# Kernel tuning notes

Hardware: AMD Instinct MI355X
Metric: run time of the kernel (lower is better)

## Reference

```python
import jax, jax.numpy as jnp
import numpy as np

B, S, H_SZ = 1, 2048, 2048
E, K, KVH, D = 8, 2, 16, 128      # experts, top_k, kv heads, head_dim
QH = K * KVH                       # 32 query heads
QSZ = KVH * D                      # 2048 per-expert q/o size


def setup_inputs() -> dict:
    key = jax.random.key(0)
    ks = jax.random.split(key, 6)
    hidden_states = jax.random.normal(ks[0], (B, S, H_SZ), jnp.float32)
    causal = jnp.tril(jnp.ones((S, S), dtype=bool))
    attention_bias = jnp.where(causal, 0.0, -1e9).astype(jnp.float32)[None, None]  # [1,1,S,S]
    inv_freq = 1.0 / (10000.0 ** (jnp.arange(0, D, 2, dtype=jnp.float32) / D))     # [D/2]
    ang = jnp.arange(S, dtype=jnp.float32)[:, None] * inv_freq[None, :]            # [S,D/2]
    cos, sin = jnp.cos(ang), jnp.sin(ang)
    router_w = jax.random.normal(ks[1], (E, H_SZ), jnp.float32) * 0.02
    q_w = jax.random.normal(ks[2], (E, QSZ, H_SZ), jnp.float32) * 0.02
    o_w = jax.random.normal(ks[3], (E, H_SZ, QSZ), jnp.float32) * 0.02
    kv_w = jax.random.normal(ks[4], (2 * QSZ, H_SZ), jnp.float32) * 0.02
    bias = jax.random.normal(ks[5], (H_SZ,), jnp.float32) * 0.02
    return {"hidden_states": hidden_states, "attention_bias": attention_bias,
            "cos": cos, "sin": sin, "router_w": router_w, "q_w": q_w,
            "o_w": o_w, "kv_w": kv_w, "bias": bias}


def _rope(x, cos, sin):
    # x: [b,s,h,d]; half-rotation rotary, cos/sin: [s,d/2]
    d2 = x.shape[-1] // 2
    x1, x2 = x[..., :d2], x[..., d2:]
    c = cos[None, :, None, :]
    s = sin[None, :, None, :]
    return jnp.concatenate([x1 * c - x2 * s, x1 * s + x2 * c], axis=-1)


def reference(hidden_states, attention_bias, cos, sin, router_w, q_w, o_w, kv_w, bias):
    # ---- router: top-k + softmax over top-k logits ----
    logits = jnp.einsum('bsh,eh->bse', hidden_states, router_w)         # [b,s,E]
    top_vals, sel = jax.lax.top_k(logits, K)                            # [b,s,K]
    gates = jax.nn.softmax(top_vals, axis=-1)                           # [b,s,K]
    # ---- per-expert Q projections (dense, as in original), gather selected ----
    q_all = jnp.einsum('bsh,eqh->bseq', hidden_states, q_w)             # [b,s,E,QSZ]
    q_sel = jnp.take_along_axis(q_all, sel[..., None], axis=2)          # [b,s,K,QSZ]
    # slots -> kv-major head layout: [b,s,K,KVH,D] -> [b,s,KVH,K,D] -> [b,s,QH,D]
    q = q_sel.reshape(B, S, K, KVH, D).transpose(0, 1, 3, 2, 4).reshape(B, S, QH, D)
    # ---- shared K/V ----
    kv = jnp.einsum('bsh,oh->bso', hidden_states, kv_w)                 # [b,s,2*QSZ]
    k_st, v_st = jnp.split(kv, 2, axis=-1)
    k_st = k_st.reshape(B, S, KVH, D)
    v_st = v_st.reshape(B, S, KVH, D)
    # ---- rotary ----
    q = _rope(q, cos, sin)
    k_st = _rope(k_st, cos, sin)
    # ---- GQA attention (group size K; kv-major query layout matches repeat) ----
    k_rep = jnp.repeat(k_st, K, axis=2)                                 # [b,s,QH,D]
    v_rep = jnp.repeat(v_st, K, axis=2)
    scale = D ** -0.5
    scores = jnp.einsum('bqhd,bkhd->bhqk', q, k_rep) * scale + attention_bias
    probs = jax.nn.softmax(scores, axis=-1)
    attn = jnp.einsum('bhqk,bkhd->bqhd', probs, v_rep)                  # [b,s,QH,D]
    # back to slot-major: [b,s,KVH,K,D] -> [b,s,K,KVH,D] -> [b,s,K,QSZ]
    attn4 = attn.reshape(B, S, KVH, K, D).transpose(0, 1, 3, 2, 4).reshape(B, S, K, QSZ)
    # ---- per-expert O projections, masked + gated sum (as in original) ----
    out = jnp.zeros((B, S, H_SZ), hidden_states.dtype)
    for e in range(E):
        o_e = jnp.einsum('bskq,hq->bskh', attn4, o_w[e])                # [b,s,K,H]
        m = (sel == e).astype(hidden_states.dtype) * gates              # [b,s,K]
        out = out + jnp.einsum('bsk,bskh->bsh', m, o_e)
    return out + bias
```

## Files before the change

kernel.cpp:

```cpp
#include <hip/hip_runtime.h>
#include <hip/hip_bf16.h>
#include <stdint.h>

#define S_LEN 2048
#define HSZ 2048
#define NE 8
#define TOPK 2
#define NKVH 16
#define HD 128
#define NQH 32
#define QSZ 2048

typedef __attribute__((ext_vector_type(8))) __bf16 bf16x8;
typedef __attribute__((ext_vector_type(4))) float f32x4;

#define BM 128
#define BN 128
#define BK 64

__device__ __forceinline__ void gload_lds16(const void* g, void* l) {
  __builtin_amdgcn_global_load_lds((__attribute__((address_space(1))) void*)g,
                                   (__attribute__((address_space(3))) void*)l, 16, 0, 0);
}

__device__ __forceinline__ bf16x8 pack8(float4 a, float4 b) {
  bf16x8 r;
  r[0] = (__bf16)a.x; r[1] = (__bf16)a.y; r[2] = (__bf16)a.z; r[3] = (__bf16)a.w;
  r[4] = (__bf16)b.x; r[5] = (__bf16)b.y; r[6] = (__bf16)b.z; r[7] = (__bf16)b.w;
  return r;
}

__global__ __launch_bounds__(256) void cast_kernel(const float* __restrict__ src,
                                                   __bf16* __restrict__ dst, long n) {
  long i0 = ((long)blockIdx.x * 256 + threadIdx.x) * 4;
  long stride = (long)gridDim.x * 256 * 4;
  for (long i = i0; i < n; i += stride) {
    float4 v = *(const float4*)(src + i);
    unsigned short a = __builtin_bit_cast(unsigned short, (__bf16)v.x);
    unsigned short b = __builtin_bit_cast(unsigned short, (__bf16)v.y);
    unsigned short c = __builtin_bit_cast(unsigned short, (__bf16)v.z);
    unsigned short d = __builtin_bit_cast(unsigned short, (__bf16)v.w);
    uint2 o;
    o.x = (unsigned)a | ((unsigned)b << 16);
    o.y = (unsigned)c | ((unsigned)d << 16);
    *(uint2*)(dst + i) = o;
  }
}

__global__ __launch_bounds__(256) void router_kernel(const float* __restrict__ hs,
                                                     const float* __restrict__ rw,
                                                     int* __restrict__ sel,
                                                     float* __restrict__ gates) {
  const int s = blockIdx.x * 4 + (threadIdx.x >> 6);
  const int lane = threadIdx.x & 63;
  const float* row = hs + (size_t)s * HSZ;
  float acc[NE];
#pragma unroll
  for (int e = 0; e < NE; ++e) acc[e] = 0.f;
  for (int j = lane; j < HSZ; j += 64) {
    float x = row[j];
#pragma unroll
    for (int e = 0; e < NE; ++e) acc[e] += x * rw[e * HSZ + j];
  }
#pragma unroll
  for (int e = 0; e < NE; ++e) {
#pragma unroll
    for (int off = 32; off > 0; off >>= 1) acc[e] += __shfl_xor(acc[e], off);
  }
  if (lane == 0) {
    int i0 = 0; float v0 = acc[0];
#pragma unroll
    for (int e = 1; e < NE; ++e) if (acc[e] > v0) { v0 = acc[e]; i0 = e; }
    int i1 = -1; float v1 = -1e30f;
#pragma unroll
    for (int e = 0; e < NE; ++e) if (e != i0 && acc[e] > v1) { v1 = acc[e]; i1 = e; }
    float ge = __expf(v1 - v0);
    float den = 1.f + ge;
    sel[s * 2] = i0; sel[s * 2 + 1] = i1;
    gates[s * 2] = 1.f / den; gates[s * 2 + 1] = ge / den;
  }
}

__global__ void bucket_kernel(const int* __restrict__ sel, int* __restrict__ pair_list,
                              int* __restrict__ expert_off) {
  __shared__ int cnt[NE], base[NE];
  const int t = threadIdx.x;
  if (t < NE) cnt[t] = 0;
  __syncthreads();
  for (int p2 = t; p2 < S_LEN * TOPK; p2 += 256) atomicAdd(&cnt[sel[p2]], 1);
  __syncthreads();
  if (t == 0) {
    int run = 0;
#pragma unroll
    for (int e = 0; e < NE; ++e) { base[e] = run; expert_off[e] = run; run += cnt[e]; }
    expert_off[NE] = run;
  }
  __syncthreads();
  for (int p2 = t; p2 < S_LEN * TOPK; p2 += 256) {
    int pos = atomicAdd(&base[sel[p2]], 1);
    pair_list[pos] = p2;
  }
}

template <int MODE>
__global__ __launch_bounds__(256) void gemm_kernel(const __bf16* __restrict__ A_src,
                                                   const float* __restrict__ B_src,
                                                   const int* __restrict__ pair_list,
                                                   const int* __restrict__ expert_off,
                                                   const float* __restrict__ gates,
                                                   __bf16* __restrict__ out_bf,
                                                   __bf16* __restrict__ out_vT,
                                                   float* __restrict__ out_f32) {
  constexpr int KD = 2048;
  constexpr int NT = KD / BK;
  const int n0 = blockIdx.x * BN;
  const int m0 = blockIdx.y * BM;
  const int e = blockIdx.z;
  int start = 0, cntv = S_LEN;
  if constexpr (MODE != 0) {
    start = expert_off[e];
    cntv = expert_off[e + 1] - start;
    if (m0 >= cntv) return;
  }
  const float* Bb = B_src + (size_t)e * QSZ * HSZ;
  __shared__ __attribute__((aligned(16))) __bf16 As[2][BM * BK];
  __shared__ __attribute__((aligned(16))) __bf16 Bs[2][BN * BK];
  __shared__ const __bf16* a_rows[BM];
  __shared__ int row_pair[BM];
  const int t = threadIdx.x;
  if (t < BM) {
    if constexpr (MODE == 0) {
      a_rows[t] = A_src + (size_t)(m0 + t) * KD;
      row_pair[t] = 0;
    } else {
      int idx = m0 + t;
      bool valid = idx < cntv;
      int pp = pair_list[start + (valid ? idx : 0)];
      row_pair[t] = valid ? pp : -1;
      size_t arow = (MODE == 1) ? (size_t)(pp >> 1) : (size_t)pp;
      a_rows[t] = A_src + arow * (size_t)KD;
    }
  }
  __syncthreads();

  const int lane = t & 63, w = t >> 6;
  const int wr = (w >> 1) * 64, wc = (w & 1) * 64;
  const int lr = lane & 15, g = lane >> 4;
  const int xa = lr & 7;

  const __bf16* a_srow[4];
  int a_soff[4];
#pragma unroll
  for (int i = 0; i < 4; ++i) {
    const int c = t + i * 256;
    const int row = c >> 3, win = c & 7;
    a_srow[i] = a_rows[row];
    a_soff[i] = (win ^ (row & 7)) * 8;
  }

  const int brow = t >> 2;
  const int bq = t & 3;
  const float* bp0 = Bb + (size_t)(n0 + brow) * KD + bq * 16;
  const float* bp1 = bp0 + (size_t)64 * KD;
  const int c0 = (2 * bq) ^ (brow & 7);
  const int c1 = (2 * bq + 1) ^ (brow & 7);
  const int bo00 = brow * BK + c0 * 8, bo01 = brow * BK + c1 * 8;
  const int bo10 = (brow + 64) * BK + c0 * 8, bo11 = (brow + 64) * BK + c1 * 8;

  f32x4 acc[4][4];
#pragma unroll
  for (int m = 0; m < 4; ++m)
#pragma unroll
    for (int n = 0; n < 4; ++n) acc[m][n] = (f32x4)0.f;

#pragma unroll
  for (int i = 0; i < 4; ++i)
    gload_lds16(a_srow[i] + a_soff[i], (char*)As[0] + (t + i * 256) * 16);
  float4 cA0 = *(const float4*)(bp0), cA1 = *(const float4*)(bp0 + 4);
  float4 cA2 = *(const float4*)(bp0 + 8), cA3 = *(const float4*)(bp0 + 12);
  float4 cB0 = *(const float4*)(bp1), cB1 = *(const float4*)(bp1 + 4);
  float4 cB2 = *(const float4*)(bp1 + 8), cB3 = *(const float4*)(bp1 + 12);

#pragma unroll 2
  for (int ti = 0; ti < NT; ++ti) {
    const int cur = ti & 1;
    *(bf16x8*)(&Bs[cur][bo00]) = pack8(cA0, cA1);
    *(bf16x8*)(&Bs[cur][bo01]) = pack8(cA2, cA3);
    *(bf16x8*)(&Bs[cur][bo10]) = pack8(cB0, cB1);
    *(bf16x8*)(&Bs[cur][bo11]) = pack8(cB2, cB3);
    __syncthreads();

    if (ti + 1 < NT) {
      const int k1 = (ti + 1) * BK;
#pragma unroll
      for (int i = 0; i < 4; ++i)
        gload_lds16(a_srow[i] + k1 + a_soff[i], (char*)As[cur ^ 1] + (t + i * 256) * 16);
      cA0 = *(const float4*)(bp0 + k1); cA1 = *(const float4*)(bp0 + k1 + 4);
      cA2 = *(const float4*)(bp0 + k1 + 8); cA3 = *(const float4*)(bp0 + k1 + 12);
      cB0 = *(const float4*)(bp1 + k1); cB1 = *(const float4*)(bp1 + k1 + 4);
      cB2 = *(const float4*)(bp1 + k1 + 8); cB3 = *(const float4*)(bp1 + k1 + 12);
    }
    __builtin_amdgcn_sched_barrier(0);

#pragma unroll
    for (int kk = 0; kk < BK; kk += 32) {
      bf16x8 af[4], bfv[4];
#pragma unroll
      for (int m = 0; m < 4; ++m)
        af[m] = *(const bf16x8*)(&As[cur][(wr + m * 16 + lr) * BK + (((kk >> 3) + g) ^ xa) * 8]);
#pragma unroll
      for (int n = 0; n < 4; ++n)
        bfv[n] = *(const bf16x8*)(&Bs[cur][(wc + n * 16 + lr) * BK + (((kk >> 3) + g) ^ xa) * 8]);
#pragma unroll
      for (int m = 0; m < 4; ++m)
#pragma unroll
        for (int n = 0; n < 4; ++n)
          acc[m][n] = __builtin_amdgcn_mfma_f32_16x16x32_bf16(af[m], bfv[n], acc[m][n], 0, 0, 0);
    }
    __builtin_amdgcn_sched_barrier(0);
  }

  const int lg = lane >> 4;
  if constexpr (MODE == 0) {
    if (n0 < 2048) {
#pragma unroll
      for (int m = 0; m < 4; ++m)
#pragma unroll
        for (int r = 0; r < 4; ++r) {
          const int row = wr + m * 16 + lg * 4 + r;
#pragma unroll
          for (int n = 0; n < 4; ++n) {
            const int col = n0 + wc + n * 16 + lr;
            out_bf[(size_t)(m0 + row) * 2048 + col] = (__bf16)acc[m][n][r];
          }
        }
    } else {
#pragma unroll
      for (int m = 0; m < 4; ++m) {
        const int sb = m0 + wr + m * 16 + lg * 4;
#pragma unroll
        for (int n = 0; n < 4; ++n) {
          const int cv = n0 + wc + n * 16 + lr - 2048;
          uint2 pk;
          unsigned short h0 = __builtin_bit_cast(unsigned short, (__bf16)acc[m][n][0]);
          unsigned short h1 = __builtin_bit_cast(unsigned short, (__bf16)acc[m][n][1]);
          unsigned short h2 = __builtin_bit_cast(unsigned short, (__bf16)acc[m][n][2]);
          unsigned short h3 = __builtin_bit_cast(unsigned short, (__bf16)acc[m][n][3]);
          pk.x = (unsigned)h0 | ((unsigned)h1 << 16);
          pk.y = (unsigned)h2 | ((unsigned)h3 << 16);
          *(uint2*)(out_vT + (size_t)cv * S_LEN + sb) = pk;
        }
      }
    }
  } else {
#pragma unroll
    for (int m = 0; m < 4; ++m) {
#pragma unroll
      for (int r = 0; r < 4; ++r) {
        const int row = wr + m * 16 + lg * 4 + r;
        const int pp = row_pair[row];
        if (pp < 0) continue;
        if constexpr (MODE == 1) {
#pragma unroll
          for (int n = 0; n < 4; ++n) {
            const int col = n0 + wc + n * 16 + lr;
            out_bf[(size_t)pp * QSZ + col] = (__bf16)acc[m][n][r];
          }
        } else {
          const float gt = gates[pp];
#pragma unroll
          for (int n = 0; n < 4; ++n) {
            const int col = n0 + wc + n * 16 + lr;
            out_f32[(size_t)pp * HSZ + col] = acc[m][n][r] * gt;
          }
        }
      }
    }
  }
}

__global__ __launch_bounds__(256) void rope_q_kernel(const __bf16* __restrict__ q_lin,
                                                     const float* __restrict__ cosb,
                                                     const float* __restrict__ sinb,
                                                     __bf16* __restrict__ q_attn) {
  const int idx = blockIdx.x * 4 + (threadIdx.x >> 6);
  const int lane = threadIdx.x & 63;
  const int s = idx >> 5;
  const int h = idx & 31;
  const int kvh = h >> 1, k = h & 1;
  const __bf16* src = q_lin + ((size_t)s * 2 + k) * QSZ + kvh * HD;
  float x1 = (float)src[lane];
  float x2 = (float)src[lane + 64];
  float c = cosb[s * 64 + lane], sn = sinb[s * 64 + lane];
  __bf16* dst = q_attn + ((size_t)h * S_LEN + s) * HD;
  dst[lane] = (__bf16)(x1 * c - x2 * sn);
  dst[lane + 64] = (__bf16)(x1 * sn + x2 * c);
}

__global__ __launch_bounds__(256) void rope_k_kernel(const __bf16* __restrict__ kv_lin,
                                                     const float* __restrict__ cosb,
                                                     const float* __restrict__ sinb,
                                                     __bf16* __restrict__ k_attn) {
  const int idx = blockIdx.x * 4 + (threadIdx.x >> 6);
  const int lane = threadIdx.x & 63;
  const int s = idx >> 4;
  const int gq = idx & 15;
  const __bf16* ksrc = kv_lin + (size_t)s * 2048 + gq * HD;
  float x1 = (float)ksrc[lane], x2 = (float)ksrc[lane + 64];
  float c = cosb[s * 64 + lane], sn = sinb[s * 64 + lane];
  __bf16* kd = k_attn + ((size_t)gq * S_LEN + s) * HD;
  kd[lane] = (__bf16)(x1 * c - x2 * sn);
  kd[lane + 64] = (__bf16)(x1 * sn + x2 * c);
}

__global__ __launch_bounds__(256, 2) void attn_kernel(const __bf16* __restrict__ q_attn,
                                                      const __bf16* __restrict__ k_attn,
                                                      const __bf16* __restrict__ vT,
                                                      __bf16* __restrict__ attn4) {
  __shared__ __attribute__((aligned(16))) __bf16 Ks[2][64 * 128];
  __shared__ __attribute__((aligned(16))) __bf16 Vs[2][128 * 64];
  const int h = blockIdx.x;
  const int by = (blockIdx.y < 8) ? blockIdx.y : 23 - blockIdx.y;
  const int s0 = by * 128;
  const int t = threadIdx.x;
  const int lane = t & 63;
  const int w = t >> 6;
  const int g = lane >> 4;
  const int lr = lane & 15;
  const int kvh = h >> 1;

  int koff[4], voff[4];
#pragma unroll
  for (int i = 0; i < 4; ++i) {
    const int c = t + i * 256;
    const int kvL = c >> 4, w16 = c & 15;
    koff[i] = kvL * HD + ((w16 ^ (kvL & 7)) * 8);
    const int d = c >> 3, w8 = c & 7;
    voff[i] = d * S_LEN + ((w8 ^ (d & 7)) * 8);
  }
  const __bf16* Kb = k_attn + (size_t)kvh * S_LEN * HD;
  const __bf16* Vb = vT + (size_t)kvh * HD * S_LEN;

  auto stage = [&](int buf, int kv0) {
#pragma unroll
    for (int i = 0; i < 4; ++i) {
      const int c = t + i * 256;
      gload_lds16(Kb + (size_t)kv0 * HD + koff[i], (char*)Ks[buf] + c * 16);
      gload_lds16(Vb + (size_t)kv0 + voff[i], (char*)Vs[buf] + c * 16);
    }
  };

  bf16x8 qf[2][4];
#pragma unroll
  for (int m = 0; m < 2; ++m) {
    const __bf16* qbase = q_attn + ((size_t)h * S_LEN + s0 + w * 32 + m * 16 + lr) * HD;
#pragma unroll
    for (int ds = 0; ds < 4; ++ds) qf[m][ds] = *(const bf16x8*)(qbase + ds * 32 + g * 8);
  }

  float m_run[2] = {-1e30f, -1e30f}, l_run[2] = {0.f, 0.f};
  f32x4 acc[2][8];
#pragma unroll
  for (int m = 0; m < 2; ++m)
#pragma unroll
    for (int dt = 0; dt < 8; ++dt) acc[m][dt] = (f32x4)0.f;

  const int xr = (lr & 7) << 4;
  const int nt = 2 * by + 2;
  stage(0, 0);
  for (int ti = 0; ti < nt; ++ti) {
    const int cur = ti & 1;
    const int kv0 = ti * 64;
    __syncthreads();
    if (ti + 1 < nt) stage(cur ^ 1, kv0 + 64);

    f32x4 sc[2][4];
#pragma unroll
    for (int m = 0; m < 2; ++m)
#pragma unroll
      for (int b = 0; b < 4; ++b) sc[m][b] = (f32x4)0.f;
#pragma unroll
    for (int b = 0; b < 4; ++b) {
#pragma unroll
      for (int ds = 0; ds < 4; ++ds) {
        const bf16x8 kf = *(const bf16x8*)((const char*)Ks[cur] +
            (b * 16 + lr) * 256 + ((ds * 64 + g * 16) ^ xr));
        sc[0][b] = __builtin_amdgcn_mfma_f32_16x16x32_bf16(kf, qf[0][ds], sc[0][b], 0, 0, 0);
        sc[1][b] = __builtin_amdgcn_mfma_f32_16x16x32_bf16(kf, qf[1][ds], sc[1][b], 0, 0, 0);
      }
    }

    bf16x8 paf[2][2];
#pragma unroll
    for (int m = 0; m < 2; ++m) {
      const int qrow = s0 + w * 32 + m * 16 + lr;
      float p[4][4];
      float tmax = -1e30f;
#pragma unroll
      for (int b = 0; b < 4; ++b)
#pragma unroll
        for (int r = 0; r < 4; ++r) {
          const int kv = kv0 + b * 16 + g * 4 + r;
          float v = sc[m][b][r] * 0.08838834764831845f;
          if (kv > qrow) v = -1e30f;
          p[b][r] = v;
          tmax = fmaxf(tmax, v);
        }
      tmax = fmaxf(tmax, __shfl_xor(tmax, 16));
      tmax = fmaxf(tmax, __shfl_xor(tmax, 32));
      const float m_new = fmaxf(m_run[m], tmax);
      const float alpha = __expf(m_run[m] - m_new);
      float lsum = 0.f;
#pragma unroll
      for (int b = 0; b < 4; ++b)
#pragma unroll
        for (int r = 0; r < 4; ++r) {
          p[b][r] = __expf(p[b][r] - m_new);
          lsum += p[b][r];
        }
      lsum += __shfl_xor(lsum, 16);
      lsum += __shfl_xor(lsum, 32);
      l_run[m] = l_run[m] * alpha + lsum;
      m_run[m] = m_new;

      float ar[4];
#pragma unroll
      for (int r = 0; r < 4; ++r) ar[r] = __shfl(alpha, g * 4 + r);
#pragma unroll
      for (int dt = 0; dt < 8; ++dt)
#pragma unroll
        for (int r = 0; r < 4; ++r) acc[m][dt][r] *= ar[r];

#pragma unroll
      for (int half = 0; half < 2; ++half) {
        bf16x8 af;
#pragma unroll
        for (int j = 0; j < 8; ++j) {
          const int srcl = lr + 16 * ((g & 1) * 2 + (j >> 2));
          const float va = __shfl(p[half * 2][j & 3], srcl);
          const float vb = __shfl(p[half * 2 + 1][j & 3], srcl);
          af[j] = (__bf16)((g >> 1) ? vb : va);
        }
        paf[m][half] = af;
      }
    }

#pragma unroll
    for (int dt = 0; dt < 8; ++dt) {
      const char* vrow = (const char*)Vs[cur] + (dt * 16 + lr) * 128;
      const bf16x8 v0 = *(const bf16x8*)(vrow + ((g * 16) ^ xr));
      const bf16x8 v1 = *(const bf16x8*)(vrow + ((64 + g * 16) ^ xr));
      acc[0][dt] = __builtin_amdgcn_mfma_f32_16x16x32_bf16(paf[0][0], v0, acc[0][dt], 0, 0, 0);
      acc[0][dt] = __builtin_amdgcn_mfma_f32_16x16x32_bf16(paf[0][1], v1, acc[0][dt], 0, 0, 0);
      acc[1][dt] = __builtin_amdgcn_mfma_f32_16x16x32_bf16(paf[1][0], v0, acc[1][dt], 0, 0, 0);
      acc[1][dt] = __builtin_amdgcn_mfma_f32_16x16x32_bf16(paf[1][1], v1, acc[1][dt], 0, 0, 0);
    }
  }

#pragma unroll
  for (int m = 0; m < 2; ++m) {
    const float li = 1.f / l_run[m];
    float linv[4];
#pragma unroll
    for (int r = 0; r < 4; ++r) linv[r] = __shfl(li, g * 4 + r);
#pragma unroll
    for (int dt = 0; dt < 8; ++dt)
#pragma unroll
      for (int r = 0; r < 4; ++r) {
        const int qg = s0 + w * 32 + m * 16 + g * 4 + r;
        attn4[((size_t)qg * 2 + (h & 1)) * QSZ + kvh * HD + dt * 16 + lr] =
            (__bf16)(acc[m][dt][r] * linv[r]);
      }
  }
}

__global__ __launch_bounds__(256) void final_kernel(const float* __restrict__ o_tmp,
                                                    const float* __restrict__ bias,
                                                    float* __restrict__ out) {
  const size_t i = ((size_t)blockIdx.x * 256 + threadIdx.x) * 4;
  const int s = (int)(i >> 11);
  const int hcol = (int)(i & 2047);
  float4 a = *(const float4*)(o_tmp + ((size_t)s * 2) * HSZ + hcol);
  float4 b = *(const float4*)(o_tmp + ((size_t)s * 2 + 1) * HSZ + hcol);
  float4 bb = *(const float4*)(bias + hcol);
  float4 o;
  o.x = a.x + b.x + bb.x; o.y = a.y + b.y + bb.y;
  o.z = a.z + b.z + bb.z; o.w = a.w + b.w + bb.w;
  *(float4*)(out + i) = o;
}

extern "C" void kernel_launch(void* const* d_in, const int* in_sizes, int n_in,
                              void* d_out, int out_size, void* d_ws, size_t ws_size,
                              hipStream_t stream) {
  (void)in_sizes; (void)n_in; (void)out_size; (void)ws_size;
  const float* hs = (const float*)d_in[0];
  const float* cosb = (const float*)d_in[2];
  const float* sinb = (const float*)d_in[3];
  const float* rw = (const float*)d_in[4];
  const float* qw = (const float*)d_in[5];
  const float* ow = (const float*)d_in[6];
  const float* kvw = (const float*)d_in[7];
  const float* bias = (const float*)d_in[8];
  float* outp = (float*)d_out;

  char* base = (char*)d_ws;
  size_t off = 0;
  auto take = [&](size_t bytes) {
    char* r = base + off;
    off += (bytes + 255) & ~(size_t)255;
    return r;
  };
  __bf16* hid_bf  = (__bf16*)take((size_t)S_LEN * HSZ * 2);
  __bf16* k_attn  = (__bf16*)take((size_t)NKVH * S_LEN * HD * 2);
  __bf16* v_attnT = (__bf16*)take((size_t)NKVH * HD * S_LEN * 2);
  char* bufA = take((size_t)S_LEN * 4096 * 2);
  char* bufBC = take((size_t)S_LEN * TOPK * HSZ * 4);
  int* sel = (int*)take((size_t)S_LEN * TOPK * 4);
  float* gates = (float*)take((size_t)S_LEN * TOPK * 4);
  int* pair_list = (int*)take((size_t)S_LEN * TOPK * 4);
  int* expert_off = (int*)take((size_t)(NE + 1) * 4);

  __bf16* kv_lin = (__bf16*)bufA;
  __bf16* attn4 = (__bf16*)bufA;
  __bf16* q_lin = (__bf16*)bufBC;
  __bf16* q_attn = (__bf16*)(bufBC + (size_t)16 * 1024 * 1024);
  float* o_tmp = (float*)bufBC;

  cast_kernel<<<1024, 256, 0, stream>>>(hs, hid_bf, (long)S_LEN * HSZ);
  router_kernel<<<S_LEN / 4, 256, 0, stream>>>(hs, rw, sel, gates);
  bucket_kernel<<<1, 256, 0, stream>>>(sel, pair_list, expert_off);
  gemm_kernel<0><<<dim3(4096 / BN, S_LEN / BM, 1), 256, 0, stream>>>(
      hid_bf, kvw, nullptr, nullptr, nullptr, kv_lin, v_attnT, nullptr);
  rope_k_kernel<<<S_LEN * NKVH / 4, 256, 0, stream>>>(kv_lin, cosb, sinb, k_attn);
  gemm_kernel<1><<<dim3(QSZ / BN, 32, NE), 256, 0, stream>>>(
      hid_bf, qw, pair_list, expert_off, nullptr, q_lin, nullptr, nullptr);
  rope_q_kernel<<<S_LEN * NQH / 4, 256, 0, stream>>>(q_lin, cosb, sinb, q_attn);
  attn_kernel<<<dim3(NQH, 16), 256, 0, stream>>>(q_attn, k_attn, v_attnT, attn4);
  gemm_kernel<2><<<dim3(HSZ / BN, 32, NE), 256, 0, stream>>>(
      attn4, ow, pair_list, expert_off, gates, nullptr, nullptr, o_tmp);
  final_kernel<<<(S_LEN * HSZ / 4) / 256, 256, 0, stream>>>(o_tmp, bias, outp);
}
```

Measured before the change: 428.8 us.

## Prefetch B tiles two stages ahead with explicit vmcnt waits in GEMM

Restructures the GEMM main loop so the fp32 B tiles are loaded into registers two K-steps ahead, using two register sets in a manually unrolled pair of steps. The bf16 A tile is still staged directly into LDS one step ahead. Explicit s_waitcnt vmcnt counts ensure only the data needed for the current tile has landed, and a raw s_barrier replaces __syncthreads. The kernel also gets a launch-bounds hint of two blocks per CU. The aim is to hide global-load latency behind the MFMA work, at the cost of more register pressure and fragile hand-counted wait values.

```diff
diff --git a/kernel.cpp b/kernel.cpp
--- a/kernel.cpp
+++ b/kernel.cpp
@@ -103,14 +103,14 @@
 }
 
 template <int MODE>
-__global__ __launch_bounds__(256) void gemm_kernel(const __bf16* __restrict__ A_src,
-                                                   const float* __restrict__ B_src,
-                                                   const int* __restrict__ pair_list,
-                                                   const int* __restrict__ expert_off,
-                                                   const float* __restrict__ gates,
-                                                   __bf16* __restrict__ out_bf,
-                                                   __bf16* __restrict__ out_vT,
-                                                   float* __restrict__ out_f32) {
+__global__ __launch_bounds__(256, 2) void gemm_kernel(const __bf16* __restrict__ A_src,
+                                                      const float* __restrict__ B_src,
+                                                      const int* __restrict__ pair_list,
+                                                      const int* __restrict__ expert_off,
+                                                      const float* __restrict__ gates,
+                                                      __bf16* __restrict__ out_bf,
+                                                      __bf16* __restrict__ out_vT,
+                                                      float* __restrict__ out_f32) {
   constexpr int KD = 2048;
   constexpr int NT = KD / BK;
   const int n0 = blockIdx.x * BN;
@@ -173,35 +173,12 @@
 #pragma unroll
     for (int n = 0; n < 4; ++n) acc[m][n] = (f32x4)0.f;
 
-#pragma unroll
-  for (int i = 0; i < 4; ++i)
-    gload_lds16(a_srow[i] + a_soff[i], (char*)As[0] + (t + i * 256) * 16);
-  float4 cA0 = *(const float4*)(bp0), cA1 = *(const float4*)(bp0 + 4);
-  float4 cA2 = *(const float4*)(bp0 + 8), cA3 = *(const float4*)(bp0 + 12);
-  float4 cB0 = *(const float4*)(bp1), cB1 = *(const float4*)(bp1 + 4);
-  float4 cB2 = *(const float4*)(bp1 + 8), cB3 = *(const float4*)(bp1 + 12);
-
-#pragma unroll 2
-  for (int ti = 0; ti < NT; ++ti) {
-    const int cur = ti & 1;
-    *(bf16x8*)(&Bs[cur][bo00]) = pack8(cA0, cA1);
-    *(bf16x8*)(&Bs[cur][bo01]) = pack8(cA2, cA3);
-    *(bf16x8*)(&Bs[cur][bo10]) = pack8(cB0, cB1);
-    *(bf16x8*)(&Bs[cur][bo11]) = pack8(cB2, cB3);
-    __syncthreads();
-
-    if (ti + 1 < NT) {
-      const int k1 = (ti + 1) * BK;
-#pragma unroll
-      for (int i = 0; i < 4; ++i)
-        gload_lds16(a_srow[i] + k1 + a_soff[i], (char*)As[cur ^ 1] + (t + i * 256) * 16);
-      cA0 = *(const float4*)(bp0 + k1); cA1 = *(const float4*)(bp0 + k1 + 4);
-      cA2 = *(const float4*)(bp0 + k1 + 8); cA3 = *(const float4*)(bp0 + k1 + 12);
-      cB0 = *(const float4*)(bp1 + k1); cB1 = *(const float4*)(bp1 + k1 + 4);
-      cB2 = *(const float4*)(bp1 + k1 + 8); cB3 = *(const float4*)(bp1 + k1 + 12);
-    }
-    __builtin_amdgcn_sched_barrier(0);
-
+  auto stageA = [&](int dstbuf, int k1) {
+#pragma unroll
+    for (int i = 0; i < 4; ++i)
+      gload_lds16(a_srow[i] + k1 + a_soff[i], (char*)As[dstbuf] + (t + i * 256) * 16);
+  };
+  auto mfma_tile = [&](int cur) {
 #pragma unroll
     for (int kk = 0; kk < BK; kk += 32) {
       bf16x8 af[4], bfv[4];
@@ -217,8 +194,46 @@
         for (int n = 0; n < 4; ++n)
           acc[m][n] = __builtin_amdgcn_mfma_f32_16x16x32_bf16(af[m], bfv[n], acc[m][n], 0, 0, 0);
     }
-    __builtin_amdgcn_sched_barrier(0);
-  }
+  };
+
+#define B_LOAD8(S0, S1, S2, S3, S4, S5, S6, S7, KB)                          \
+  S0 = *(const float4*)(bp0 + (KB));      S1 = *(const float4*)(bp0 + (KB) + 4);  \
+  S2 = *(const float4*)(bp0 + (KB) + 8);  S3 = *(const float4*)(bp0 + (KB) + 12); \
+  S4 = *(const float4*)(bp1 + (KB));      S5 = *(const float4*)(bp1 + (KB) + 4);  \
+  S6 = *(const float4*)(bp1 + (KB) + 8);  S7 = *(const float4*)(bp1 + (KB) + 12);
+
+#define GEMM_STEP(TI, CUR, S0, S1, S2, S3, S4, S5, S6, S7)                   \
+  *(bf16x8*)(&Bs[CUR][bo00]) = pack8(S0, S1);                                \
+  *(bf16x8*)(&Bs[CUR][bo01]) = pack8(S2, S3);                                \
+  *(bf16x8*)(&Bs[CUR][bo10]) = pack8(S4, S5);                                \
+  *(bf16x8*)(&Bs[CUR][bo11]) = pack8(S6, S7);                                \
+  asm volatile("s_waitcnt lgkmcnt(0)" ::: "memory");                         \
+  __builtin_amdgcn_s_barrier();                                              \
+  if ((TI) + 2 < NT) { B_LOAD8(S0, S1, S2, S3, S4, S5, S6, S7, ((TI) + 2) * BK) } \
+  __builtin_amdgcn_sched_barrier(0);                                         \
+  if ((TI) + 1 < NT) stageA((CUR) ^ 1, ((TI) + 1) * BK);                     \
+  __builtin_amdgcn_sched_barrier(0);                                         \
+  if ((TI) + 2 < NT) { asm volatile("s_waitcnt vmcnt(12)" ::: "memory"); }   \
+  else if ((TI) + 1 < NT) { asm volatile("s_waitcnt vmcnt(4)" ::: "memory"); } \
+  else { asm volatile("s_waitcnt vmcnt(0)" ::: "memory"); }                  \
+  __builtin_amdgcn_sched_barrier(0);                                         \
+  mfma_tile(CUR);                                                            \
+  __builtin_amdgcn_sched_barrier(0);
+
+  float4 bA0, bA1, bA2, bA3, bA4, bA5, bA6, bA7;
+  float4 bB0, bB1, bB2, bB3, bB4, bB5, bB6, bB7;
+  B_LOAD8(bA0, bA1, bA2, bA3, bA4, bA5, bA6, bA7, 0)
+  B_LOAD8(bB0, bB1, bB2, bB3, bB4, bB5, bB6, bB7, BK)
+  __builtin_amdgcn_sched_barrier(0);
+  stageA(0, 0);
+  __builtin_amdgcn_sched_barrier(0);
+
+  for (int tb = 0; tb < NT; tb += 2) {
+    GEMM_STEP(tb, 0, bA0, bA1, bA2, bA3, bA4, bA5, bA6, bA7)
+    GEMM_STEP(tb + 1, 1, bB0, bB1, bB2, bB3, bB4, bB5, bB6, bB7)
+  }
+#undef GEMM_STEP
+#undef B_LOAD8
 
   const int lg = lane >> 4;
   if constexpr (MODE == 0) {
```

After: 435.7 us. Within noise of the previous version (+1.6%).

## Shrink GEMM N-tile and drop double buffering to raise occupancy

Applied to the files above, without the earlier changes.

The tiled GEMM kernel is reworked to use 128x64 output tiles, with four waves each owning 32 rows, instead of 128x128 tiles on a 2x2 wave grid. The LDS double buffer and the register prefetch of the next K-slice are removed in favour of a plain load, sync, compute, sync loop. Launch bounds now request 4 blocks per CU. The aim is higher occupancy and more blocks to hide latency. The cost is no explicit load/compute overlap and twice the re-reads of the A tile across N tiles. The MoE grid's y-dimension is trimmed to 16, the maximum number of 128-row tiles per expert.

```diff
diff --git a/kernel.cpp b/kernel.cpp
--- a/kernel.cpp
+++ b/kernel.cpp
@@ -15,7 +15,7 @@
 typedef __attribute__((ext_vector_type(4))) float f32x4;
 
 #define BM 128
-#define BN 128
+#define BN 64
 #define BK 64
 
 __device__ __forceinline__ void gload_lds16(const void* g, void* l) {
@@ -103,14 +103,14 @@
 }
 
 template <int MODE>
-__global__ __launch_bounds__(256) void gemm_kernel(const __bf16* __restrict__ A_src,
-                                                   const float* __restrict__ B_src,
-                                                   const int* __restrict__ pair_list,
-                                                   const int* __restrict__ expert_off,
-                                                   const float* __restrict__ gates,
-                                                   __bf16* __restrict__ out_bf,
-                                                   __bf16* __restrict__ out_vT,
-                                                   float* __restrict__ out_f32) {
+__global__ __launch_bounds__(256, 4) void gemm_kernel(const __bf16* __restrict__ A_src,
+                                                      const float* __restrict__ B_src,
+                                                      const int* __restrict__ pair_list,
+                                                      const int* __restrict__ expert_off,
+                                                      const float* __restrict__ gates,
+                                                      __bf16* __restrict__ out_bf,
+                                                      __bf16* __restrict__ out_vT,
+                                                      float* __restrict__ out_f32) {
   constexpr int KD = 2048;
   constexpr int NT = KD / BK;
   const int n0 = blockIdx.x * BN;
@@ -123,8 +123,8 @@
     if (m0 >= cntv) return;
   }
   const float* Bb = B_src + (size_t)e * QSZ * HSZ;
-  __shared__ __attribute__((aligned(16))) __bf16 As[2][BM * BK];
-  __shared__ __attribute__((aligned(16))) __bf16 Bs[2][BN * BK];
+  __shared__ __attribute__((aligned(16))) __bf16 As[BM * BK];
+  __shared__ __attribute__((aligned(16))) __bf16 Bs[BN * BK];
   __shared__ const __bf16* a_rows[BM];
   __shared__ int row_pair[BM];
   const int t = threadIdx.x;
@@ -144,7 +144,7 @@
   __syncthreads();
 
   const int lane = t & 63, w = t >> 6;
-  const int wr = (w >> 1) * 64, wc = (w & 1) * 64;
+  const int wr = w * 32;
   const int lr = lane & 15, g = lane >> 4;
   const int xa = lr & 7;
 
@@ -161,86 +161,70 @@
   const int brow = t >> 2;
   const int bq = t & 3;
   const float* bp0 = Bb + (size_t)(n0 + brow) * KD + bq * 16;
-  const float* bp1 = bp0 + (size_t)64 * KD;
   const int c0 = (2 * bq) ^ (brow & 7);
   const int c1 = (2 * bq + 1) ^ (brow & 7);
-  const int bo00 = brow * BK + c0 * 8, bo01 = brow * BK + c1 * 8;
-  const int bo10 = (brow + 64) * BK + c0 * 8, bo11 = (brow + 64) * BK + c1 * 8;
-
-  f32x4 acc[4][4];
-#pragma unroll
-  for (int m = 0; m < 4; ++m)
+  const int bo0 = brow * BK + c0 * 8, bo1 = brow * BK + c1 * 8;
+
+  f32x4 acc[2][4];
+#pragma unroll
+  for (int m = 0; m < 2; ++m)
 #pragma unroll
     for (int n = 0; n < 4; ++n) acc[m][n] = (f32x4)0.f;
 
-#pragma unroll
-  for (int i = 0; i < 4; ++i)
-    gload_lds16(a_srow[i] + a_soff[i], (char*)As[0] + (t + i * 256) * 16);
-  float4 cA0 = *(const float4*)(bp0), cA1 = *(const float4*)(bp0 + 4);
-  float4 cA2 = *(const float4*)(bp0 + 8), cA3 = *(const float4*)(bp0 + 12);
-  float4 cB0 = *(const float4*)(bp1), cB1 = *(const float4*)(bp1 + 4);
-  float4 cB2 = *(const float4*)(bp1 + 8), cB3 = *(const float4*)(bp1 + 12);
-
-#pragma unroll 2
   for (int ti = 0; ti < NT; ++ti) {
-    const int cur = ti & 1;
-    *(bf16x8*)(&Bs[cur][bo00]) = pack8(cA0, cA1);
-    *(bf16x8*)(&Bs[cur][bo01]) = pack8(cA2, cA3);
-    *(bf16x8*)(&Bs[cur][bo10]) = pack8(cB0, cB1);
-    *(bf16x8*)(&Bs[cur][bo11]) = pack8(cB2, cB3);
+    const int k0 = ti * BK;
+#pragma unroll
+    for (int i = 0; i < 4; ++i)
+      gload_lds16(a_srow[i] + k0 + a_soff[i], (char*)As + (t + i * 256) * 16);
+    {
+      float4 f0 = *(const float4*)(bp0 + k0);
+      float4 f1 = *(const float4*)(bp0 + k0 + 4);
+      float4 f2 = *(const float4*)(bp0 + k0 + 8);
+      float4 f3 = *(const float4*)(bp0 + k0 + 12);
+      *(bf16x8*)(&Bs[bo0]) = pack8(f0, f1);
+      *(bf16x8*)(&Bs[bo1]) = pack8(f2, f3);
+    }
     __syncthreads();
 
-    if (ti + 1 < NT) {
-      const int k1 = (ti + 1) * BK;
-#pragma unroll
-      for (int i = 0; i < 4; ++i)
-        gload_lds16(a_srow[i] + k1 + a_soff[i], (char*)As[cur ^ 1] + (t + i * 256) * 16);
-      cA0 = *(const float4*)(bp0 + k1); cA1 = *(const float4*)(bp0 + k1 + 4);
-      cA2 = *(const float4*)(bp0 + k1 + 8); cA3 = *(const float4*)(bp0 + k1 + 12);
-      cB0 = *(const float4*)(bp1 + k1); cB1 = *(const float4*)(bp1 + k1 + 4);
-      cB2 = *(const float4*)(bp1 + k1 + 8); cB3 = *(const float4*)(bp1 + k1 + 12);
-    }
-    __builtin_amdgcn_sched_barrier(0);
-
 #pragma unroll
     for (int kk = 0; kk < BK; kk += 32) {
-      bf16x8 af[4], bfv[4];
-#pragma unroll
-      for (int m = 0; m < 4; ++m)
-        af[m] = *(const bf16x8*)(&As[cur][(wr + m * 16 + lr) * BK + (((kk >> 3) + g) ^ xa) * 8]);
+      bf16x8 af[2], bfv[4];
+#pragma unroll
+      for (int m = 0; m < 2; ++m)
+        af[m] = *(const bf16x8*)(&As[(wr + m * 16 + lr) * BK + (((kk >> 3) + g) ^ xa) * 8]);
 #pragma unroll
       for (int n = 0; n < 4; ++n)
-        bfv[n] = *(const bf16x8*)(&Bs[cur][(wc + n * 16 + lr) * BK + (((kk >> 3) + g) ^ xa) * 8]);
-#pragma unroll
-      for (int m = 0; m < 4; ++m)
+        bfv[n] = *(const bf16x8*)(&Bs[(n * 16 + lr) * BK + (((kk >> 3) + g) ^ xa) * 8]);
+#pragma unroll
+      for (int m = 0; m < 2; ++m)
 #pragma unroll
         for (int n = 0; n < 4; ++n)
           acc[m][n] = __builtin_amdgcn_mfma_f32_16x16x32_bf16(af[m], bfv[n], acc[m][n], 0, 0, 0);
     }
-    __builtin_amdgcn_sched_barrier(0);
+    __syncthreads();
   }
 
   const int lg = lane >> 4;
   if constexpr (MODE == 0) {
     if (n0 < 2048) {
 #pragma unroll
-      for (int m = 0; m < 4; ++m)
+      for (int m = 0; m < 2; ++m)
 #pragma unroll
         for (int r = 0; r < 4; ++r) {
           const int row = wr + m * 16 + lg * 4 + r;
 #pragma unroll
           for (int n = 0; n < 4; ++n) {
-            const int col = n0 + wc + n * 16 + lr;
+            const int col = n0 + n * 16 + lr;
             out_bf[(size_t)(m0 + row) * 2048 + col] = (__bf16)acc[m][n][r];
           }
         }
     } else {
 #pragma unroll
-      for (int m = 0; m < 4; ++m) {
+      for (int m = 0; m < 2; ++m) {
         const int sb = m0 + wr + m * 16 + lg * 4;
 #pragma unroll
         for (int n = 0; n < 4; ++n) {
-          const int cv = n0 + wc + n * 16 + lr - 2048;
+          const int cv = n0 + n * 16 + lr - 2048;
           uint2 pk;
           unsigned short h0 = __builtin_bit_cast(unsigned short, (__bf16)acc[m][n][0]);
           unsigned short h1 = __builtin_bit_cast(unsigned short, (__bf16)acc[m][n][1]);
@@ -254,7 +238,7 @@
     }
   } else {
 #pragma unroll
-    for (int m = 0; m < 4; ++m) {
+    for (int m = 0; m < 2; ++m) {
 #pragma unroll
       for (int r = 0; r < 4; ++r) {
         const int row = wr + m * 16 + lg * 4 + r;
@@ -263,14 +247,14 @@
         if constexpr (MODE == 1) {
 #pragma unroll
           for (int n = 0; n < 4; ++n) {
-            const int col = n0 + wc + n * 16 + lr;
+            const int col = n0 + n * 16 + lr;
             out_bf[(size_t)pp * QSZ + col] = (__bf16)acc[m][n][r];
           }
         } else {
           const float gt = gates[pp];
 #pragma unroll
           for (int n = 0; n < 4; ++n) {
-            const int col = n0 + wc + n * 16 + lr;
+            const int col = n0 + n * 16 + lr;
             out_f32[(size_t)pp * HSZ + col] = acc[m][n][r] * gt;
           }
         }
@@ -532,11 +516,11 @@
   gemm_kernel<0><<<dim3(4096 / BN, S_LEN / BM, 1), 256, 0, stream>>>(
       hid_bf, kvw, nullptr, nullptr, nullptr, kv_lin, v_attnT, nullptr);
   rope_k_kernel<<<S_LEN * NKVH / 4, 256, 0, stream>>>(kv_lin, cosb, sinb, k_attn);
-  gemm_kernel<1><<<dim3(QSZ / BN, 32, NE), 256, 0, stream>>>(
+  gemm_kernel<1><<<dim3(QSZ / BN, 16, NE), 256, 0, stream>>>(
       hid_bf, qw, pair_list, expert_off, nullptr, q_lin, nullptr, nullptr);
   rope_q_kernel<<<S_LEN * NQH / 4, 256, 0, stream>>>(q_lin, cosb, sinb, q_attn);
   attn_kernel<<<dim3(NQH, 16), 256, 0, stream>>>(q_attn, k_attn, v_attnT, attn4);
-  gemm_kernel<2><<<dim3(HSZ / BN, 32, NE), 256, 0, stream>>>(
+  gemm_kernel<2><<<dim3(HSZ / BN, 16, NE), 256, 0, stream>>>(
       attn4, ow, pair_list, expert_off, gates, nullptr, nullptr, o_tmp);
   final_kernel<<<(S_LEN * HSZ / 4) / 256, 256, 0, stream>>>(o_tmp, bias, outp);
 }
```

Measured after the change: 463.3 us. +8.0%, slower.

## Merge KV and Q GEMMs into one launch, split-K the O GEMM, single-buffer LDS

Applied to the files above, without the earlier changes.

Fuses the KV projection and the per-expert Q projection GEMMs into a single launch with a flat block index, so both run concurrently and fill the device better. The O-projection GEMM is split along K into two halves that write gated bf16 partials, and the final kernel sums four partial rows plus bias. The GEMM main loops drop the register/LDS double-buffer prefetch in favor of a single LDS buffer with two barriers per tile, and launch_bounds request 4 blocks per CU for occupancy. The trade-off is losing load/compute overlap within a block, and bf16 partials reduce accuracy of the output accumulation.

```diff
diff --git a/kernel.cpp b/kernel.cpp
--- a/kernel.cpp
+++ b/kernel.cpp
@@ -102,34 +102,40 @@
   }
 }
 
-template <int MODE>
-__global__ __launch_bounds__(256) void gemm_kernel(const __bf16* __restrict__ A_src,
-                                                   const float* __restrict__ B_src,
-                                                   const int* __restrict__ pair_list,
-                                                   const int* __restrict__ expert_off,
-                                                   const float* __restrict__ gates,
-                                                   __bf16* __restrict__ out_bf,
-                                                   __bf16* __restrict__ out_vT,
-                                                   float* __restrict__ out_f32) {
+
+__global__ __launch_bounds__(256, 4) void gemm01_kernel(
+    const __bf16* __restrict__ A_src, const float* __restrict__ kvw,
+    const float* __restrict__ qw, const int* __restrict__ pair_list,
+    const int* __restrict__ expert_off, __bf16* __restrict__ kv_lin,
+    __bf16* __restrict__ out_vT, __bf16* __restrict__ q_lin) {
   constexpr int KD = 2048;
   constexpr int NT = KD / BK;
-  const int n0 = blockIdx.x * BN;
-  const int m0 = blockIdx.y * BM;
-  const int e = blockIdx.z;
-  int start = 0, cntv = S_LEN;
-  if constexpr (MODE != 0) {
+  const int bid = blockIdx.x;
+  const bool isKV = bid < 512;
+  int n0, m0, start = 0, cntv = S_LEN;
+  const float* Bb;
+  if (isKV) {
+    n0 = (bid & 31) * BN;
+    m0 = (bid >> 5) * BM;
+    Bb = kvw;
+  } else {
+    const int rem = bid - 512;
+    const int e = rem >> 8;
+    const int r2 = rem & 255;
+    n0 = (r2 & 15) * BN;
+    m0 = (r2 >> 4) * BM;
     start = expert_off[e];
     cntv = expert_off[e + 1] - start;
     if (m0 >= cntv) return;
-  }
-  const float* Bb = B_src + (size_t)e * QSZ * HSZ;
-  __shared__ __attribute__((aligned(16))) __bf16 As[2][BM * BK];
-  __shared__ __attribute__((aligned(16))) __bf16 Bs[2][BN * BK];
+    Bb = qw + (size_t)e * QSZ * HSZ;
+  }
+  __shared__ __attribute__((aligned(16))) __bf16 As[BM * BK];
+  __shared__ __attribute__((aligned(16))) __bf16 Bs[BN * BK];
   __shared__ const __bf16* a_rows[BM];
   __shared__ int row_pair[BM];
   const int t = threadIdx.x;
   if (t < BM) {
-    if constexpr (MODE == 0) {
+    if (isKV) {
       a_rows[t] = A_src + (size_t)(m0 + t) * KD;
       row_pair[t] = 0;
     } else {
@@ -137,8 +143,7 @@
       bool valid = idx < cntv;
       int pp = pair_list[start + (valid ? idx : 0)];
       row_pair[t] = valid ? pp : -1;
-      size_t arow = (MODE == 1) ? (size_t)(pp >> 1) : (size_t)pp;
-      a_rows[t] = A_src + arow * (size_t)KD;
+      a_rows[t] = A_src + (size_t)(pp >> 1) * KD;
     }
   }
   __syncthreads();
@@ -158,14 +163,11 @@
     a_soff[i] = (win ^ (row & 7)) * 8;
   }
 
-  const int brow = t >> 2;
-  const int bq = t & 3;
-  const float* bp0 = Bb + (size_t)(n0 + brow) * KD + bq * 16;
-  const float* bp1 = bp0 + (size_t)64 * KD;
-  const int c0 = (2 * bq) ^ (brow & 7);
-  const int c1 = (2 * bq + 1) ^ (brow & 7);
-  const int bo00 = brow * BK + c0 * 8, bo01 = brow * BK + c1 * 8;
-  const int bo10 = (brow + 64) * BK + c0 * 8, bo11 = (brow + 64) * BK + c1 * 8;
+  const int br = t >> 1, bh = t & 1;
+  const float* bp = Bb + (size_t)(n0 + br) * KD + bh * 32;
+  int bo[4];
+#pragma unroll
+  for (int j = 0; j < 4; ++j) bo[j] = br * BK + (((bh * 4 + j) ^ (br & 7)) * 8);
 
   f32x4 acc[4][4];
 #pragma unroll
@@ -173,55 +175,38 @@
 #pragma unroll
     for (int n = 0; n < 4; ++n) acc[m][n] = (f32x4)0.f;
 
-#pragma unroll
-  for (int i = 0; i < 4; ++i)
-    gload_lds16(a_srow[i] + a_soff[i], (char*)As[0] + (t + i * 256) * 16);
-  float4 cA0 = *(const float4*)(bp0), cA1 = *(const float4*)(bp0 + 4);
-  float4 cA2 = *(const float4*)(bp0 + 8), cA3 = *(const float4*)(bp0 + 12);
-  float4 cB0 = *(const float4*)(bp1), cB1 = *(const float4*)(bp1 + 4);
-  float4 cB2 = *(const float4*)(bp1 + 8), cB3 = *(const float4*)(bp1 + 12);
-
-#pragma unroll 2
   for (int ti = 0; ti < NT; ++ti) {
-    const int cur = ti & 1;
-    *(bf16x8*)(&Bs[cur][bo00]) = pack8(cA0, cA1);
-    *(bf16x8*)(&Bs[cur][bo01]) = pack8(cA2, cA3);
-    *(bf16x8*)(&Bs[cur][bo10]) = pack8(cB0, cB1);
-    *(bf16x8*)(&Bs[cur][bo11]) = pack8(cB2, cB3);
+    const int k0 = ti * BK;
+#pragma unroll
+    for (int i = 0; i < 4; ++i)
+      gload_lds16(a_srow[i] + k0 + a_soff[i], (char*)As + (t + i * 256) * 16);
+#pragma unroll
+    for (int j = 0; j < 4; ++j) {
+      float4 fa = *(const float4*)(bp + k0 + j * 8);
+      float4 fb = *(const float4*)(bp + k0 + j * 8 + 4);
+      *(bf16x8*)(&Bs[bo[j]]) = pack8(fa, fb);
+    }
     __syncthreads();
-
-    if (ti + 1 < NT) {
-      const int k1 = (ti + 1) * BK;
-#pragma unroll
-      for (int i = 0; i < 4; ++i)
-        gload_lds16(a_srow[i] + k1 + a_soff[i], (char*)As[cur ^ 1] + (t + i * 256) * 16);
-      cA0 = *(const float4*)(bp0 + k1); cA1 = *(const float4*)(bp0 + k1 + 4);
-      cA2 = *(const float4*)(bp0 + k1 + 8); cA3 = *(const float4*)(bp0 + k1 + 12);
-      cB0 = *(const float4*)(bp1 + k1); cB1 = *(const float4*)(bp1 + k1 + 4);
-      cB2 = *(const float4*)(bp1 + k1 + 8); cB3 = *(const float4*)(bp1 + k1 + 12);
-    }
-    __builtin_amdgcn_sched_barrier(0);
-
 #pragma unroll
     for (int kk = 0; kk < BK; kk += 32) {
       bf16x8 af[4], bfv[4];
 #pragma unroll
       for (int m = 0; m < 4; ++m)
-        af[m] = *(const bf16x8*)(&As[cur][(wr + m * 16 + lr) * BK + (((kk >> 3) + g) ^ xa) * 8]);
+        af[m] = *(const bf16x8*)(&As[(wr + m * 16 + lr) * BK + (((kk >> 3) + g) ^ xa) * 8]);
 #pragma unroll
       for (int n = 0; n < 4; ++n)
-        bfv[n] = *(const bf16x8*)(&Bs[cur][(wc + n * 16 + lr) * BK + (((kk >> 3) + g) ^ xa) * 8]);
+        bfv[n] = *(const bf16x8*)(&Bs[(wc + n * 16 + lr) * BK + (((kk >> 3) + g) ^ xa) * 8]);
 #pragma unroll
       for (int m = 0; m < 4; ++m)
 #pragma unroll
         for (int n = 0; n < 4; ++n)
           acc[m][n] = __builtin_amdgcn_mfma_f32_16x16x32_bf16(af[m], bfv[n], acc[m][n], 0, 0, 0);
     }
-    __builtin_amdgcn_sched_barrier(0);
+    __syncthreads();
   }
 
   const int lg = lane >> 4;
-  if constexpr (MODE == 0) {
+  if (isKV) {
     if (n0 < 2048) {
 #pragma unroll
       for (int m = 0; m < 4; ++m)
@@ -231,7 +216,7 @@
 #pragma unroll
           for (int n = 0; n < 4; ++n) {
             const int col = n0 + wc + n * 16 + lr;
-            out_bf[(size_t)(m0 + row) * 2048 + col] = (__bf16)acc[m][n][r];
+            kv_lin[(size_t)(m0 + row) * 2048 + col] = (__bf16)acc[m][n][r];
           }
         }
     } else {
@@ -260,20 +245,119 @@
         const int row = wr + m * 16 + lg * 4 + r;
         const int pp = row_pair[row];
         if (pp < 0) continue;
-        if constexpr (MODE == 1) {
-#pragma unroll
-          for (int n = 0; n < 4; ++n) {
-            const int col = n0 + wc + n * 16 + lr;
-            out_bf[(size_t)pp * QSZ + col] = (__bf16)acc[m][n][r];
-          }
-        } else {
-          const float gt = gates[pp];
-#pragma unroll
-          for (int n = 0; n < 4; ++n) {
-            const int col = n0 + wc + n * 16 + lr;
-            out_f32[(size_t)pp * HSZ + col] = acc[m][n][r] * gt;
-          }
+#pragma unroll
+        for (int n = 0; n < 4; ++n) {
+          const int col = n0 + wc + n * 16 + lr;
+          q_lin[(size_t)pp * QSZ + col] = (__bf16)acc[m][n][r];
         }
+      }
+    }
+  }
+}
+
+__global__ __launch_bounds__(256, 4) void gemm2_kernel(
+    const __bf16* __restrict__ A_src, const float* __restrict__ ow,
+    const int* __restrict__ pair_list, const int* __restrict__ expert_off,
+    const float* __restrict__ gates, __bf16* __restrict__ o_part) {
+  constexpr int KD = 2048;
+  constexpr int NT = 16;
+  const int bid = blockIdx.x;
+  const int kz = bid >> 11;
+  const int rem = bid & 2047;
+  const int e = rem >> 8;
+  const int r2 = rem & 255;
+  const int n0 = (r2 & 15) * BN;
+  const int m0 = (r2 >> 4) * BM;
+  const int start = expert_off[e];
+  const int cntv = expert_off[e + 1] - start;
+  if (m0 >= cntv) return;
+  const int kbase = kz * 1024;
+  const float* Bb = ow + (size_t)e * HSZ * QSZ;
+
+  __shared__ __attribute__((aligned(16))) __bf16 As[BM * BK];
+  __shared__ __attribute__((aligned(16))) __bf16 Bs[BN * BK];
+  __shared__ const __bf16* a_rows[BM];
+  __shared__ int row_pair[BM];
+  const int t = threadIdx.x;
+  if (t < BM) {
+    int idx = m0 + t;
+    bool valid = idx < cntv;
+    int pp = pair_list[start + (valid ? idx : 0)];
+    row_pair[t] = valid ? pp : -1;
+    a_rows[t] = A_src + (size_t)pp * KD + kbase;
+  }
+  __syncthreads();
+
+  const int lane = t & 63, w = t >> 6;
+  const int wr = (w >> 1) * 64, wc = (w & 1) * 64;
+  const int lr = lane & 15, g = lane >> 4;
+  const int xa = lr & 7;
+
+  const __bf16* a_srow[4];
+  int a_soff[4];
+#pragma unroll
+  for (int i = 0; i < 4; ++i) {
+    const int c = t + i * 256;
+    const int row = c >> 3, win = c & 7;
+    a_srow[i] = a_rows[row];
+    a_soff[i] = (win ^ (row & 7)) * 8;
+  }
+
+  const int br = t >> 1, bh = t & 1;
+  const float* bp = Bb + (size_t)(n0 + br) * KD + kbase + bh * 32;
+  int bo[4];
+#pragma unroll
+  for (int j = 0; j < 4; ++j) bo[j] = br * BK + (((bh * 4 + j) ^ (br & 7)) * 8);
+
+  f32x4 acc[4][4];
+#pragma unroll
+  for (int m = 0; m < 4; ++m)
+#pragma unroll
+    for (int n = 0; n < 4; ++n) acc[m][n] = (f32x4)0.f;
+
+  for (int ti = 0; ti < NT; ++ti) {
+    const int k0 = ti * BK;
+#pragma unroll
+    for (int i = 0; i < 4; ++i)
+      gload_lds16(a_srow[i] + k0 + a_soff[i], (char*)As + (t + i * 256) * 16);
+#pragma unroll
+    for (int j = 0; j < 4; ++j) {
+      float4 fa = *(const float4*)(bp + k0 + j * 8);
+      float4 fb = *(const float4*)(bp + k0 + j * 8 + 4);
+      *(bf16x8*)(&Bs[bo[j]]) = pack8(fa, fb);
+    }
+    __syncthreads();
+#pragma unroll
+    for (int kk = 0; kk < BK; kk += 32) {
+      bf16x8 af[4], bfv[4];
+#pragma unroll
+      for (int m = 0; m < 4; ++m)
+        af[m] = *(const bf16x8*)(&As[(wr + m * 16 + lr) * BK + (((kk >> 3) + g) ^ xa) * 8]);
+#pragma unroll
+      for (int n = 0; n < 4; ++n)
+        bfv[n] = *(const bf16x8*)(&Bs[(wc + n * 16 + lr) * BK + (((kk >> 3) + g) ^ xa) * 8]);
+#pragma unroll
+      for (int m = 0; m < 4; ++m)
+#pragma unroll
+        for (int n = 0; n < 4; ++n)
+          acc[m][n] = __builtin_amdgcn_mfma_f32_16x16x32_bf16(af[m], bfv[n], acc[m][n], 0, 0, 0);
+    }
+    __syncthreads();
+  }
+
+  const int lg = lane >> 4;
+#pragma unroll
+  for (int m = 0; m < 4; ++m) {
+#pragma unroll
+    for (int r = 0; r < 4; ++r) {
+      const int row = wr + m * 16 + lg * 4 + r;
+      const int pp = row_pair[row];
+      if (pp < 0) continue;
+      const float gt = gates[pp];
+#pragma unroll
+      for (int n = 0; n < 4; ++n) {
+        const int col = n0 + wc + n * 16 + lr;
+        o_part[((size_t)kz * 4096 + pp) * HSZ + col] = (__bf16)(acc[m][n][r] * gt);
       }
     }
   }
@@ -474,19 +558,23 @@
   }
 }
 
-__global__ __launch_bounds__(256) void final_kernel(const float* __restrict__ o_tmp,
+__global__ __launch_bounds__(256) void final_kernel(const __bf16* __restrict__ o_part,
                                                     const float* __restrict__ bias,
                                                     float* __restrict__ out) {
   const size_t i = ((size_t)blockIdx.x * 256 + threadIdx.x) * 4;
   const int s = (int)(i >> 11);
   const int hcol = (int)(i & 2047);
-  float4 a = *(const float4*)(o_tmp + ((size_t)s * 2) * HSZ + hcol);
-  float4 b = *(const float4*)(o_tmp + ((size_t)s * 2 + 1) * HSZ + hcol);
-  float4 bb = *(const float4*)(bias + hcol);
-  float4 o;
-  o.x = a.x + b.x + bb.x; o.y = a.y + b.y + bb.y;
-  o.z = a.z + b.z + bb.z; o.w = a.w + b.w + bb.w;
-  *(float4*)(out + i) = o;
+  float4 r = *(const float4*)(bias + hcol);
+#pragma unroll
+  for (int idx = 0; idx < 4; ++idx) {
+    const size_t row = (size_t)(idx >> 1) * 4096 + 2 * s + (idx & 1);
+    const ushort4 u = *(const ushort4*)(o_part + row * HSZ + hcol);
+    r.x += (float)__builtin_bit_cast(__bf16, u.x);
+    r.y += (float)__builtin_bit_cast(__bf16, u.y);
+    r.z += (float)__builtin_bit_cast(__bf16, u.z);
+    r.w += (float)__builtin_bit_cast(__bf16, u.w);
+  }
+  *(float4*)(out + i) = r;
 }
 
 extern "C" void kernel_launch(void* const* d_in, const int* in_sizes, int n_in,
@@ -514,7 +602,7 @@
   __bf16* k_attn  = (__bf16*)take((size_t)NKVH * S_LEN * HD * 2);
   __bf16* v_attnT = (__bf16*)take((size_t)NKVH * HD * S_LEN * 2);
   char* bufA = take((size_t)S_LEN * 4096 * 2);
-  char* bufBC = take((size_t)S_LEN * TOPK * HSZ * 4);
+  char* bufBC = take((size_t)2 * 4096 * HSZ * 2);
   int* sel = (int*)take((size_t)S_LEN * TOPK * 4);
   float* gates = (float*)take((size_t)S_LEN * TOPK * 4);
   int* pair_list = (int*)take((size_t)S_LEN * TOPK * 4);
@@ -524,19 +612,17 @@
   __bf16* attn4 = (__bf16*)bufA;
   __bf16* q_lin = (__bf16*)bufBC;
   __bf16* q_attn = (__bf16*)(bufBC + (size_t)16 * 1024 * 1024);
-  float* o_tmp = (float*)bufBC;
+  __bf16* o_part = (__bf16*)bufBC;
 
   cast_kernel<<<1024, 256, 0, stream>>>(hs, hid_bf, (long)S_LEN * HSZ);
   router_kernel<<<S_LEN / 4, 256, 0, stream>>>(hs, rw, sel, gates);
   bucket_kernel<<<1, 256, 0, stream>>>(sel, pair_list, expert_off);
-  gemm_kernel<0><<<dim3(4096 / BN, S_LEN / BM, 1), 256, 0, stream>>>(
-      hid_bf, kvw, nullptr, nullptr, nullptr, kv_lin, v_attnT, nullptr);
+  gemm01_kernel<<<512 + NE * 256, 256, 0, stream>>>(
+      hid_bf, kvw, qw, pair_list, expert_off, kv_lin, v_attnT, q_lin);
   rope_k_kernel<<<S_LEN * NKVH / 4, 256, 0, stream>>>(kv_lin, cosb, sinb, k_attn);
-  gemm_kernel<1><<<dim3(QSZ / BN, 32, NE), 256, 0, stream>>>(
-      hid_bf, qw, pair_list, expert_off, nullptr, q_lin, nullptr, nullptr);
   rope_q_kernel<<<S_LEN * NQH / 4, 256, 0, stream>>>(q_lin, cosb, sinb, q_attn);
   attn_kernel<<<dim3(NQH, 16), 256, 0, stream>>>(q_attn, k_attn, v_attnT, attn4);
-  gemm_kernel<2><<<dim3(HSZ / BN, 32, NE), 256, 0, stream>>>(
-      attn4, ow, pair_list, expert_off, gates, nullptr, nullptr, o_tmp);
-  final_kernel<<<(S_LEN * HSZ / 4) / 256, 256, 0, stream>>>(o_tmp, bias, outp);
-}
+  gemm2_kernel<<<2 * NE * 256, 256, 0, stream>>>(
+      attn4, ow, pair_list, expert_off, gates, o_part);
+  final_kernel<<<(S_LEN * HSZ / 4) / 256, 256, 0, stream>>>(o_part, bias, outp);
+}
```

After: 516.7 us. 20.5% more time.
